# Performance work log

Hardware: AMD Instinct MI355X
Metric: run time of the kernel (lower is better)

Reference implementation:

```python
import jax, jax.numpy as jnp
import numpy as np

N_NODES = 100000
N_EDGES = 1600000
NFEAT, NHID, NCLASS = 256, 512, 256


def _init_params(key):
    ks = jax.random.split(key, 8)
    s = 0.02
    p = {
        'W1a': jax.random.normal(ks[0], (NFEAT, NHID), jnp.float32) * s,
        'b1a': jnp.zeros((NHID,), jnp.float32),
        'W1b': jax.random.normal(ks[1], (NHID, NHID), jnp.float32) * s,
        'b1b': jnp.zeros((NHID,), jnp.float32),
        'W2a': jax.random.normal(ks[2], (NHID, NHID), jnp.float32) * s,
        'b2a': jnp.zeros((NHID,), jnp.float32),
        'W2b': jax.random.normal(ks[3], (NHID, NCLASS), jnp.float32) * s,
        'b2b': jnp.zeros((NCLASS,), jnp.float32),
        'eps1': jnp.zeros((), jnp.float32),
        'eps2': jnp.zeros((), jnp.float32),
    }
    return p


def setup_inputs() -> dict:
    key = jax.random.key(0)
    kx, ke, kp = jax.random.split(key, 3)
    x = jax.random.normal(kx, (N_NODES, NFEAT), jnp.float32)
    edge_index = jax.random.randint(ke, (2, N_EDGES), 0, N_NODES, jnp.int64)
    inp = {'x': x, 'edge_index': edge_index}
    inp.update(_init_params(kp))
    return inp


def _gin_agg(h, src, dst, eps, n_nodes):
    # sum of neighbor (source) features at each destination node + (1+eps)*self
    agg = jax.ops.segment_sum(h[src], dst, num_segments=n_nodes)
    return (1.0 + eps) * h + agg


def reference(x, edge_index, W1a, b1a, W1b, b1b, W2a, b2a, W2b, b2b, eps1, eps2):
    src, dst = edge_index[0], edge_index[1]
    n = x.shape[0]
    # GINConv layer 1: MLP = Linear-ReLU-Linear-ReLU
    h = _gin_agg(x, src, dst, eps1, n)
    h = jax.nn.relu(h @ W1a + b1a)
    h = jax.nn.relu(h @ W1b + b1b)
    # dropout: eval mode (identity)
    # GINConv layer 2: MLP = Linear-ReLU-Linear
    h = _gin_agg(h, src, dst, eps2, n)
    h = jax.nn.relu(h @ W2a + b2a)
    out = h @ W2b + b2b
    return out
```

## Files before the change

### kernel.cpp

```cpp
#include <hip/hip_runtime.h>
#include <hip/hip_bf16.h>
#include <stdint.h>

#define NN 100000
#define NFEATD 256
#define NHIDD 512
#define NCLASSD 256

typedef short bf16x8 __attribute__((ext_vector_type(8)));
typedef float f32x4 __attribute__((ext_vector_type(4)));
typedef float f32x2 __attribute__((ext_vector_type(2)));

__device__ __forceinline__ float bf2f(uint32_t u) {
    union { uint32_t i; float f; } v; v.i = u << 16; return v.f;
}
__device__ __forceinline__ ushort f2bf(float f) {
    uint32_t x = __float_as_uint(f);
    uint32_t r = (x + 0x7FFF + ((x >> 16) & 1)) >> 16;
    return (ushort)r;
}

__global__ void zero_i32(int* __restrict__ p, int n) {
    int i = blockIdx.x * 256 + threadIdx.x;
    if (i < n) p[i] = 0;
}

__global__ void count_deg(const int* __restrict__ dst, int* __restrict__ deg, int nE) {
    int e = blockIdx.x * 256 + threadIdx.x;
    if (e < nE) atomicAdd(&deg[dst[e]], 1);
}

__global__ __launch_bounds__(1024) void scan_excl(const int* __restrict__ deg,
                                                  int* __restrict__ off, int n) {
    __shared__ int wsum[16];
    __shared__ int carry_s;
    const int tid = threadIdx.x;
    const int lane = tid & 63, wv = tid >> 6;
    if (tid == 0) carry_s = 0;
    __syncthreads();
    for (int base = 0; base < n; base += 1024) {
        int i = base + tid;
        int v = (i < n) ? deg[i] : 0;
        int x = v;
#pragma unroll
        for (int d = 1; d < 64; d <<= 1) {
            int y = __shfl_up(x, d, 64);
            if (lane >= d) x += y;
        }
        if (lane == 63) wsum[wv] = x;
        __syncthreads();
        if (wv == 0 && lane < 16) {
            int s = wsum[lane];
#pragma unroll
            for (int d = 1; d < 16; d <<= 1) {
                int y = __shfl_up(s, d, 16);
                if (lane >= d) s += y;
            }
            wsum[lane] = s;
        }
        __syncthreads();
        int carry = carry_s;
        int wprefix = (wv == 0) ? 0 : wsum[wv - 1];
        if (i < n) off[i] = carry + wprefix + x - v;
        __syncthreads();
        if (tid == 0) carry_s = carry + wsum[15];
        __syncthreads();
    }
    if (tid == 0) off[n] = carry_s;
}

__global__ void fill_csr(const int* __restrict__ src, const int* __restrict__ dst,
                         const int* __restrict__ off, int* __restrict__ cursor,
                         int* __restrict__ csr, int nE) {
    int e = blockIdx.x * 256 + threadIdx.x;
    if (e >= nE) return;
    int d = dst[e];
    int p = off[d] + atomicAdd(&cursor[d], 1);
    csr[p] = src[e];
}

__global__ void prep_w(const float* __restrict__ W, ushort* __restrict__ Wt, int K, int N) {
    int idx = blockIdx.x * 256 + threadIdx.x;
    if (idx >= K * N) return;
    int k = idx / N, n = idx - k * N;
    Wt[(size_t)n * K + k] = f2bf(W[idx]);
}

__global__ void cast_f32_fp8(const float* __restrict__ a, uint8_t* __restrict__ o, int n) {
    int i = (blockIdx.x * 256 + threadIdx.x) * 8;
    if (i >= n) return;
    float4 v0 = *(const float4*)(a + i);
    float4 v1 = *(const float4*)(a + i + 4);
    int lo = __builtin_amdgcn_cvt_pk_fp8_f32(v0.x, v0.y, 0, false);
    lo = __builtin_amdgcn_cvt_pk_fp8_f32(v0.z, v0.w, lo, true);
    int hi = __builtin_amdgcn_cvt_pk_fp8_f32(v1.x, v1.y, 0, false);
    hi = __builtin_amdgcn_cvt_pk_fp8_f32(v1.z, v1.w, hi, true);
    uint2 r; r.x = (uint32_t)lo; r.y = (uint32_t)hi;
    *(uint2*)(o + i) = r;
}

__device__ __forceinline__ void acc4_fp8(uint32_t p, float w, float& a0, float& a1,
                                         float& a2, float& a3) {
    f32x2 u = __builtin_amdgcn_cvt_pk_f32_fp8((int)p, false);
    f32x2 v = __builtin_amdgcn_cvt_pk_f32_fp8((int)p, true);
    a0 += w * u[0]; a1 += w * u[1]; a2 += w * v[0]; a3 += w * v[1];
}

__global__ void gather256f8(const uint8_t* __restrict__ X8, const int* __restrict__ off,
                            const int* __restrict__ csr, const float* __restrict__ eps,
                            ushort* __restrict__ out) {
    int node = (blockIdx.x * 256 + threadIdx.x) >> 6;
    if (node >= NN) return;
    int lane = threadIdx.x & 63;
    float sc = 1.0f + *eps;
    const uint32_t* X1 = (const uint32_t*)X8;
    float a0 = 0, a1 = 0, a2 = 0, a3 = 0;
    acc4_fp8(X1[(size_t)node * 64 + lane], sc, a0, a1, a2, a3);
    int e = off[node], e1 = off[node + 1];
    for (; e + 3 < e1; e += 4) {
        int s0 = csr[e], s1 = csr[e + 1], s2 = csr[e + 2], s3 = csr[e + 3];
        uint32_t p0 = X1[(size_t)s0 * 64 + lane];
        uint32_t p1 = X1[(size_t)s1 * 64 + lane];
        uint32_t p2 = X1[(size_t)s2 * 64 + lane];
        uint32_t p3 = X1[(size_t)s3 * 64 + lane];
        acc4_fp8(p0, 1.f, a0, a1, a2, a3);
        acc4_fp8(p1, 1.f, a0, a1, a2, a3);
        acc4_fp8(p2, 1.f, a0, a1, a2, a3);
        acc4_fp8(p3, 1.f, a0, a1, a2, a3);
    }
    for (; e < e1; ++e)
        acc4_fp8(X1[(size_t)csr[e] * 64 + lane], 1.f, a0, a1, a2, a3);
    uint2 r;
    r.x = (uint32_t)f2bf(a0) | ((uint32_t)f2bf(a1) << 16);
    r.y = (uint32_t)f2bf(a2) | ((uint32_t)f2bf(a3) << 16);
    *(uint2*)(out + (size_t)node * 256 + lane * 4) = r;
}

__global__ void gather512f8(const uint8_t* __restrict__ H8, const int* __restrict__ off,
                            const int* __restrict__ csr, const float* __restrict__ eps,
                            ushort* __restrict__ out) {
    int node = (blockIdx.x * 256 + threadIdx.x) >> 6;
    if (node >= NN) return;
    int lane = threadIdx.x & 63;
    float sc = 1.0f + *eps;
    const uint2* H2 = (const uint2*)H8;
    float a0 = 0, a1 = 0, a2 = 0, a3 = 0, a4 = 0, a5 = 0, a6 = 0, a7 = 0;
    {
        uint2 p = H2[(size_t)node * 64 + lane];
        acc4_fp8(p.x, sc, a0, a1, a2, a3);
        acc4_fp8(p.y, sc, a4, a5, a6, a7);
    }
    int e = off[node], e1 = off[node + 1];
    for (; e + 3 < e1; e += 4) {
        int s0 = csr[e], s1 = csr[e + 1], s2 = csr[e + 2], s3 = csr[e + 3];
        uint2 p0 = H2[(size_t)s0 * 64 + lane];
        uint2 p1 = H2[(size_t)s1 * 64 + lane];
        uint2 p2 = H2[(size_t)s2 * 64 + lane];
        uint2 p3 = H2[(size_t)s3 * 64 + lane];
        acc4_fp8(p0.x, 1.f, a0, a1, a2, a3); acc4_fp8(p0.y, 1.f, a4, a5, a6, a7);
        acc4_fp8(p1.x, 1.f, a0, a1, a2, a3); acc4_fp8(p1.y, 1.f, a4, a5, a6, a7);
        acc4_fp8(p2.x, 1.f, a0, a1, a2, a3); acc4_fp8(p2.y, 1.f, a4, a5, a6, a7);
        acc4_fp8(p3.x, 1.f, a0, a1, a2, a3); acc4_fp8(p3.y, 1.f, a4, a5, a6, a7);
    }
    for (; e < e1; ++e) {
        uint2 p0 = H2[(size_t)csr[e] * 64 + lane];
        acc4_fp8(p0.x, 1.f, a0, a1, a2, a3);
        acc4_fp8(p0.y, 1.f, a4, a5, a6, a7);
    }
    uint4 r;
    r.x = (uint32_t)f2bf(a0) | ((uint32_t)f2bf(a1) << 16);
    r.y = (uint32_t)f2bf(a2) | ((uint32_t)f2bf(a3) << 16);
    r.z = (uint32_t)f2bf(a4) | ((uint32_t)f2bf(a5) << 16);
    r.w = (uint32_t)f2bf(a6) | ((uint32_t)f2bf(a7) << 16);
    *(uint4*)(out + (size_t)node * 512 + lane * 8) = r;
}

__global__ __launch_bounds__(256) void gemm_bt(
    const ushort* __restrict__ A, const ushort* __restrict__ Bt,
    const float* __restrict__ bias, float* __restrict__ outf,
    uint8_t* __restrict__ out8, ushort* __restrict__ outb,
    int M, int N, int K, int relu)
{
    __shared__ ushort As[128 * 32];
    __shared__ ushort Bs[128 * 32];
    const int tid = threadIdx.x;
    const int wave = tid >> 6, lane = tid & 63;
    const int quad = lane >> 4, lrow = lane & 15;
    const int wr = wave >> 1, wc = wave & 1;
    const int row0 = blockIdx.x * 128, col0 = blockIdx.y * 128;

    f32x4 acc[4][4] = {};

    for (int k0 = 0; k0 < K; k0 += 32) {
#pragma unroll
        for (int it = 0; it < 2; ++it) {
            int chunk = it * 256 + tid;
            int r = chunk >> 2, c = chunk & 3;
            int gr = row0 + r; if (gr > M - 1) gr = M - 1;
            const ushort* gp = A + (size_t)gr * K + (k0 + c * 8);
            __builtin_amdgcn_global_load_lds((const __attribute__((address_space(1))) void*)gp,
                (__attribute__((address_space(3))) void*)(As + chunk * 8), 16, 0, 0);
        }
#pragma unroll
        for (int it = 0; it < 2; ++it) {
            int chunk = it * 256 + tid;
            int r = chunk >> 2, c = chunk & 3;
            const ushort* gp = Bt + (size_t)(col0 + r) * K + (k0 + c * 8);
            __builtin_amdgcn_global_load_lds((const __attribute__((address_space(1))) void*)gp,
                (__attribute__((address_space(3))) void*)(Bs + chunk * 8), 16, 0, 0);
        }
        __syncthreads();

        bf16x8 af[4], bfr[4];
#pragma unroll
        for (int i = 0; i < 4; ++i)
            af[i] = *(const bf16x8*)(As + (wr * 64 + i * 16 + lrow) * 32 + quad * 8);
#pragma unroll
        for (int j = 0; j < 4; ++j)
            bfr[j] = *(const bf16x8*)(Bs + (wc * 64 + j * 16 + lrow) * 32 + quad * 8);
#pragma unroll
        for (int i = 0; i < 4; ++i)
#pragma unroll
            for (int j = 0; j < 4; ++j)
                acc[i][j] = __builtin_amdgcn_mfma_f32_16x16x32_bf16(af[i], bfr[j], acc[i][j], 0, 0, 0);
        __syncthreads();
    }

#pragma unroll
    for (int i = 0; i < 4; ++i) {
        int rbase = row0 + wr * 64 + i * 16 + quad * 4;
#pragma unroll
        for (int j = 0; j < 4; ++j) {
            int c = col0 + wc * 64 + j * 16 + lrow;
            float bv = bias[c];
#pragma unroll
            for (int g = 0; g < 4; ++g) {
                int rr = rbase + g;
                if (rr < M) {
                    float v = acc[i][j][g] + bv;
                    if (relu) v = fmaxf(v, 0.f);
                    if (outf) outf[(size_t)rr * N + c] = v;
                    else if (out8) {
                        int enc = __builtin_amdgcn_cvt_pk_fp8_f32(v, v, 0, false);
                        out8[(size_t)rr * N + c] = (uint8_t)(enc & 0xff);
                    }
                    else outb[(size_t)rr * N + c] = f2bf(v);
                }
            }
        }
    }
}

extern "C" void kernel_launch(void* const* d_in, const int* in_sizes, int n_in,
                              void* d_out, int out_size, void* d_ws, size_t ws_size,
                              hipStream_t stream) {
    const float* x    = (const float*)d_in[0];
    const int*   ei   = (const int*)d_in[1];
    const float* W1a  = (const float*)d_in[2];
    const float* b1a  = (const float*)d_in[3];
    const float* W1b  = (const float*)d_in[4];
    const float* b1b  = (const float*)d_in[5];
    const float* W2a  = (const float*)d_in[6];
    const float* b2a  = (const float*)d_in[7];
    const float* W2b  = (const float*)d_in[8];
    const float* b2b  = (const float*)d_in[9];
    const float* eps1 = (const float*)d_in[10];
    const float* eps2 = (const float*)d_in[11];
    const int nE = in_sizes[1] / 2;
    const int* srcv = ei;
    const int* dstv = ei + nE;

    char* ws = (char*)d_ws;
    int*    off    = (int*)(ws);
    int*    cursor = (int*)(ws + 524288);
    int*    csr    = (int*)(ws + 1048576);
    ushort* Wt1a   = (ushort*)(ws + 8388608);
    ushort* Wt1b   = Wt1a + 512 * 256;
    ushort* Wt2a   = Wt1b + 512 * 512;
    ushort* Wt2b   = Wt2a + 512 * 512;
    char*   P      = ws + 10485760;
    char*   Q      = ws + 10485760 + 102400000;
    uint8_t* x8    = (uint8_t*)P;
    ushort* agg1b  = (ushort*)Q;
    ushort* h1     = (ushort*)P;
    uint8_t* h2f8  = (uint8_t*)Q;
    ushort* agg2b  = (ushort*)P;
    ushort* h3     = (ushort*)Q;

    zero_i32<<<(NN + 255) / 256, 256, 0, stream>>>(cursor, NN);
    count_deg<<<(nE + 255) / 256, 256, 0, stream>>>(dstv, cursor, nE);
    scan_excl<<<1, 1024, 0, stream>>>(cursor, off, NN);
    zero_i32<<<(NN + 255) / 256, 256, 0, stream>>>(cursor, NN);
    fill_csr<<<(nE + 255) / 256, 256, 0, stream>>>(srcv, dstv, off, cursor, csr, nE);

    prep_w<<<(NFEATD * NHIDD + 255) / 256, 256, 0, stream>>>(W1a, Wt1a, NFEATD, NHIDD);
    prep_w<<<(NHIDD * NHIDD + 255) / 256, 256, 0, stream>>>(W1b, Wt1b, NHIDD, NHIDD);
    prep_w<<<(NHIDD * NHIDD + 255) / 256, 256, 0, stream>>>(W2a, Wt2a, NHIDD, NHIDD);
    prep_w<<<(NHIDD * NCLASSD + 255) / 256, 256, 0, stream>>>(W2b, Wt2b, NHIDD, NCLASSD);
    cast_f32_fp8<<<(NN * NFEATD / 8 + 255) / 256, 256, 0, stream>>>(x, x8, NN * NFEATD);

    gather256f8<<<(NN * 64) / 256, 256, 0, stream>>>(x8, off, csr, eps1, agg1b);
    dim3 g1((NN + 127) / 128, NHIDD / 128);
    gemm_bt<<<g1, 256, 0, stream>>>(agg1b, Wt1a, b1a, nullptr, nullptr, h1, NN, NHIDD, NFEATD, 1);
    gemm_bt<<<g1, 256, 0, stream>>>(h1, Wt1b, b1b, nullptr, h2f8, nullptr, NN, NHIDD, NHIDD, 1);

    gather512f8<<<(NN * 64) / 256, 256, 0, stream>>>(h2f8, off, csr, eps2, agg2b);
    gemm_bt<<<g1, 256, 0, stream>>>(agg2b, Wt2a, b2a, nullptr, nullptr, h3, NN, NHIDD, NHIDD, 1);
    dim3 g2((NN + 127) / 128, NCLASSD / 128);
    gemm_bt<<<g2, 256, 0, stream>>>(h3, Wt2b, b2b, (float*)d_out, nullptr, nullptr, NN, NCLASSD, NHIDD, 0);
}
```

Measured before the change: 1.027 ms.

## Replace 128x128 GEMM with 256x256 tile, 4-stage LDS pipeline and split barriers

```diff
diff --git a/kernel.cpp b/kernel.cpp
--- a/kernel.cpp
+++ b/kernel.cpp
@@ -19,6 +19,10 @@
     uint32_t r = (x + 0x7FFF + ((x >> 16) & 1)) >> 16;
     return (ushort)r;
 }
+
+#define FENCE() asm volatile("" ::: "memory")
+#define BARRIER() do { FENCE(); __builtin_amdgcn_s_barrier(); FENCE(); } while (0)
+#define VMCNT(n) asm volatile("s_waitcnt vmcnt(" #n ")" ::: "memory")
 
 __global__ void zero_i32(int* __restrict__ p, int n) {
     int i = blockIdx.x * 256 + threadIdx.x;
@@ -175,69 +179,92 @@
     *(uint4*)(out + (size_t)node * 512 + lane * 8) = r;
 }
 
-__global__ __launch_bounds__(256) void gemm_bt(
+
+__device__ __forceinline__ void stage16(const ushort* __restrict__ G, int ldk,
+                                        int grow0, int kc, ushort* dst, int tid, int rclamp) {
+#pragma unroll
+    for (int i = 0; i < 2; ++i) {
+        int u = i * 512 + tid;
+        int r = u >> 2, cblk = u & 3;
+        int gr = grow0 + r; if (gr > rclamp) gr = rclamp;
+        const ushort* gp = G + (size_t)gr * ldk + kc + cblk * 8;
+        __builtin_amdgcn_global_load_lds((const __attribute__((address_space(1))) void*)gp,
+            (__attribute__((address_space(3))) void*)(dst + (size_t)u * 8), 16, 0, 0);
+    }
+}
+
+__global__ __launch_bounds__(512, 2) void gemm256(
     const ushort* __restrict__ A, const ushort* __restrict__ Bt,
     const float* __restrict__ bias, float* __restrict__ outf,
     uint8_t* __restrict__ out8, ushort* __restrict__ outb,
     int M, int N, int K, int relu)
 {
-    __shared__ ushort As[128 * 32];
-    __shared__ ushort Bs[128 * 32];
+    extern __shared__ ushort smem[];
     const int tid = threadIdx.x;
     const int wave = tid >> 6, lane = tid & 63;
     const int quad = lane >> 4, lrow = lane & 15;
-    const int wr = wave >> 1, wc = wave & 1;
-    const int row0 = blockIdx.x * 128, col0 = blockIdx.y * 128;
-
-    f32x4 acc[4][4] = {};
-
-    for (int k0 = 0; k0 < K; k0 += 32) {
-#pragma unroll
-        for (int it = 0; it < 2; ++it) {
-            int chunk = it * 256 + tid;
-            int r = chunk >> 2, c = chunk & 3;
-            int gr = row0 + r; if (gr > M - 1) gr = M - 1;
-            const ushort* gp = A + (size_t)gr * K + (k0 + c * 8);
-            __builtin_amdgcn_global_load_lds((const __attribute__((address_space(1))) void*)gp,
-                (__attribute__((address_space(3))) void*)(As + chunk * 8), 16, 0, 0);
-        }
-#pragma unroll
-        for (int it = 0; it < 2; ++it) {
-            int chunk = it * 256 + tid;
-            int r = chunk >> 2, c = chunk & 3;
-            const ushort* gp = Bt + (size_t)(col0 + r) * K + (k0 + c * 8);
-            __builtin_amdgcn_global_load_lds((const __attribute__((address_space(1))) void*)gp,
-                (__attribute__((address_space(3))) void*)(Bs + chunk * 8), 16, 0, 0);
-        }
-        __syncthreads();
-
-        bf16x8 af[4], bfr[4];
-#pragma unroll
-        for (int i = 0; i < 4; ++i)
-            af[i] = *(const bf16x8*)(As + (wr * 64 + i * 16 + lrow) * 32 + quad * 8);
-#pragma unroll
-        for (int j = 0; j < 4; ++j)
-            bfr[j] = *(const bf16x8*)(Bs + (wc * 64 + j * 16 + lrow) * 32 + quad * 8);
-#pragma unroll
-        for (int i = 0; i < 4; ++i)
-#pragma unroll
-            for (int j = 0; j < 4; ++j)
-                acc[i][j] = __builtin_amdgcn_mfma_f32_16x16x32_bf16(af[i], bfr[j], acc[i][j], 0, 0, 0);
-        __syncthreads();
-    }
-
-#pragma unroll
-    for (int i = 0; i < 4; ++i) {
-        int rbase = row0 + wr * 64 + i * 16 + quad * 4;
-#pragma unroll
-        for (int j = 0; j < 4; ++j) {
-            int c = col0 + wc * 64 + j * 16 + lrow;
-            float bv = bias[c];
+    const int wr = wave >> 2, wcn = wave & 3;
+    const int row0 = blockIdx.y * 256, col0 = blockIdx.x * 256;
+    const int NC = K >> 5;
+
+    f32x4 acc[8][4] = {};
+
+    stage16(A,  K, row0, 0,  smem,                tid, M - 1);
+    stage16(Bt, K, col0, 0,  smem + 8192,         tid, N - 1);
+    stage16(A,  K, row0, 32, smem + 16384,        tid, M - 1);
+    stage16(Bt, K, col0, 32, smem + 16384 + 8192, tid, N - 1);
+
+    for (int j = 0; j < NC; ++j) {
+        const ushort* sA = smem + (j & 3) * 16384;
+        const ushort* sB = sA + 8192;
+        ushort* nslot = smem + ((j + 2) & 3) * 16384;
+        bf16x8 af[4], bf[4];
+
+        if (j + 2 < NC) stage16(A, K, row0, (j + 2) << 5, nslot, tid, M - 1);
+        if (j + 2 < NC)      { VMCNT(6); }
+        else if (j + 1 < NC) { VMCNT(4); }
+        else                 { VMCNT(0); }
+        BARRIER();
+#pragma unroll
+        for (int m = 0; m < 4; ++m)
+            af[m] = *(const bf16x8*)(sA + (wr * 128 + m * 16 + lrow) * 32 + quad * 8);
+#pragma unroll
+        for (int n = 0; n < 4; ++n)
+            bf[n] = *(const bf16x8*)(sB + (wcn * 64 + n * 16 + lrow) * 32 + quad * 8);
+        __builtin_amdgcn_s_setprio(1);
+#pragma unroll
+        for (int m = 0; m < 4; ++m)
+#pragma unroll
+            for (int n = 0; n < 4; ++n)
+                acc[m][n] = __builtin_amdgcn_mfma_f32_16x16x32_bf16(af[m], bf[n], acc[m][n], 0, 0, 0);
+        __builtin_amdgcn_s_setprio(0);
+
+        if (j + 2 < NC) stage16(Bt, K, col0, (j + 2) << 5, nslot + 8192, tid, N - 1);
+        BARRIER();
+#pragma unroll
+        for (int m = 0; m < 4; ++m)
+            af[m] = *(const bf16x8*)(sA + (wr * 128 + (m + 4) * 16 + lrow) * 32 + quad * 8);
+        __builtin_amdgcn_s_setprio(1);
+#pragma unroll
+        for (int m = 0; m < 4; ++m)
+#pragma unroll
+            for (int n = 0; n < 4; ++n)
+                acc[m + 4][n] = __builtin_amdgcn_mfma_f32_16x16x32_bf16(af[m], bf[n], acc[m + 4][n], 0, 0, 0);
+        __builtin_amdgcn_s_setprio(0);
+    }
+
+#pragma unroll
+    for (int n = 0; n < 4; ++n) {
+        int c = col0 + wcn * 64 + n * 16 + lrow;
+        float bv = bias[c];
+#pragma unroll
+        for (int m = 0; m < 8; ++m) {
+            int rbase = row0 + wr * 128 + m * 16 + quad * 4;
 #pragma unroll
             for (int g = 0; g < 4; ++g) {
                 int rr = rbase + g;
                 if (rr < M) {
-                    float v = acc[i][j][g] + bv;
+                    float v = acc[m][n][g] + bv;
                     if (relu) v = fmaxf(v, 0.f);
                     if (outf) outf[(size_t)rr * N + c] = v;
                     else if (out8) {
@@ -270,6 +297,13 @@
     const int* srcv = ei;
     const int* dstv = ei + nE;
 
+    static int s_attr_done = 0;
+    if (!s_attr_done) {
+        hipFuncSetAttribute((const void*)gemm256,
+                            hipFuncAttributeMaxDynamicSharedMemorySize, 131072);
+        s_attr_done = 1;
+    }
+
     char* ws = (char*)d_ws;
     int*    off    = (int*)(ws);
     int*    cursor = (int*)(ws + 524288);
@@ -300,12 +334,12 @@
     cast_f32_fp8<<<(NN * NFEATD / 8 + 255) / 256, 256, 0, stream>>>(x, x8, NN * NFEATD);
 
     gather256f8<<<(NN * 64) / 256, 256, 0, stream>>>(x8, off, csr, eps1, agg1b);
-    dim3 g1((NN + 127) / 128, NHIDD / 128);
-    gemm_bt<<<g1, 256, 0, stream>>>(agg1b, Wt1a, b1a, nullptr, nullptr, h1, NN, NHIDD, NFEATD, 1);
-    gemm_bt<<<g1, 256, 0, stream>>>(h1, Wt1b, b1b, nullptr, h2f8, nullptr, NN, NHIDD, NHIDD, 1);
+    dim3 g1(NHIDD / 256, (NN + 255) / 256);
+    gemm256<<<g1, 512, 131072, stream>>>(agg1b, Wt1a, b1a, nullptr, nullptr, h1, NN, NHIDD, NFEATD, 1);
+    gemm256<<<g1, 512, 131072, stream>>>(h1, Wt1b, b1b, nullptr, h2f8, nullptr, NN, NHIDD, NHIDD, 1);
 
     gather512f8<<<(NN * 64) / 256, 256, 0, stream>>>(h2f8, off, csr, eps2, agg2b);
-    gemm_bt<<<g1, 256, 0, stream>>>(agg2b, Wt2a, b2a, nullptr, nullptr, h3, NN, NHIDD, NHIDD, 1);
-    dim3 g2((NN + 127) / 128, NCLASSD / 128);
-    gemm_bt<<<g2, 256, 0, stream>>>(h3, Wt2b, b2b, (float*)d_out, nullptr, nullptr, NN, NCLASSD, NHIDD, 0);
-}
+    gemm256<<<g1, 512, 131072, stream>>>(agg2b, Wt2a, b2a, nullptr, nullptr, h3, NN, NHIDD, NHIDD, 1);
+    dim3 g2(NCLASSD / 256, (NN + 255) / 256);
+    gemm256<<<g2, 512, 131072, stream>>>(h3, Wt2b, b2b, (float*)d_out, nullptr, nullptr, NN, NCLASSD, NHIDD, 0);
+}
```

Measured after the change: 1.121 ms. +9.2%, slower.
